# Kernel tuning notes

Hardware: AMD Instinct MI355X
Metric: run time of the kernel (lower is better)

Reference implementation:

```python
import jax, jax.numpy as jnp
import numpy as np

DIM = 512
HEADS = 8
SEQ = 2048
BATCH = 4


def setup_inputs() -> dict:
    key = jax.random.key(0)
    k = jax.random.split(key, 6)
    x = jax.random.normal(k[0], (BATCH, SEQ, DIM), dtype=jnp.float32)
    mask = jax.random.normal(k[1], (BATCH, SEQ, SEQ), dtype=jnp.float32)
    Wqkv = jax.random.normal(k[2], (3 * DIM, DIM), dtype=jnp.float32) * 0.02
    Btab = jax.random.normal(k[3], (1, HEADS, 2 * SEQ - 1), dtype=jnp.float32) * 0.02
    Wproj = jax.random.normal(k[4], (DIM, DIM), dtype=jnp.float32) * 0.02
    bproj = jax.random.normal(k[5], (DIM,), dtype=jnp.float32) * 0.02
    return {"x": x, "mask": mask, "Wqkv": Wqkv, "Btab": Btab,
            "Wproj": Wproj, "bproj": bproj}


def reference(x, mask, Wqkv, Btab, Wproj, bproj):
    B, N, C = x.shape
    H = Btab.shape[1]
    seq = (Btab.shape[2] + 1) // 2
    head_dim = C // H
    scale = head_dim ** (-0.5)

    # qkv projection (no bias), split into q,k,v of shape [B,H,N,head_dim]
    qkv = (x @ Wqkv.T).reshape(B, N, 3, H, head_dim)
    qkv = jnp.transpose(qkv, (2, 0, 3, 1, 4))  # [3,B,H,N,hd]
    q, k, v = qkv[0], qkv[1], qkv[2]

    # gathered relative-position bias: B_index[i,j] = i - j + seq - 1
    idx = jnp.arange(N)[:, None] - jnp.arange(N)[None, :] + (seq - 1)  # [N,N]
    bias = Btab[:, :, idx]  # [1,H,N,N]

    attn = jnp.einsum('bhnd,bhmd->bhnm', q, k) * scale + bias
    attn = attn + mask[:, None, :, :]  # additive mask, broadcast over heads
    attn = jax.nn.softmax(attn, axis=-1)

    out = jnp.einsum('bhnm,bhmd->bhnd', attn, v)  # [B,H,N,hd]
    out = jnp.transpose(out, (0, 2, 1, 3)).reshape(B, N, C)
    return out @ Wproj.T + bproj
```

## Files before the change

kernel.cpp:

```cpp
#include <hip/hip_runtime.h>


typedef __attribute__((ext_vector_type(8))) short short8;
typedef __attribute__((ext_vector_type(4))) float f32x4;

#define SEQ   2048
#define NHEAD 8
#define NBATCH 4
#define HD    64
#define CDIM  512

__device__ __forceinline__ unsigned short f32_to_bf16_rn(float f) {
  unsigned u = __builtin_bit_cast(unsigned, f);
  u += 0x7FFFu + ((u >> 16) & 1u);
  return (unsigned short)(u >> 16);
}

__global__ __launch_bounds__(256) void cvt_f32_bf16(const float* __restrict__ in,
                                                    ushort* __restrict__ out, int n4) {
  int i = blockIdx.x * 256 + threadIdx.x;
  const int stride = gridDim.x * 256;
  for (; i < n4; i += stride) {
    float4 v = reinterpret_cast<const float4*>(in)[i];
    ushort4 o;
    o.x = f32_to_bf16_rn(v.x);
    o.y = f32_to_bf16_rn(v.y);
    o.z = f32_to_bf16_rn(v.z);
    o.w = f32_to_bf16_rn(v.w);
    reinterpret_cast<ushort4*>(out)[i] = o;
  }
}

template <int MODE>
__global__ __launch_bounds__(256) void gemm_nt(
    const ushort* __restrict__ A, const ushort* __restrict__ Bm,
    ushort* __restrict__ qo, ushort* __restrict__ ko, ushort* __restrict__ vto,
    const float* __restrict__ bias, float* __restrict__ outf) {
  const int K = 512;
  __shared__ ushort As[128 * 40];
  __shared__ ushort Bs[128 * 40];

  const int t = threadIdx.x;
  const int bn = blockIdx.x, bm = blockIdx.y;
  const int lane = t & 63, w = t >> 6;
  const int wm = w >> 1, wn = w & 1;
  const int lr = lane & 15, lq = lane >> 4;
  const int m0 = bm * 128, n0 = bn * 128;

  f32x4 acc[4][4];
#pragma unroll
  for (int i = 0; i < 4; ++i)
#pragma unroll
    for (int j = 0; j < 4; ++j) acc[i][j] = (f32x4){0.f, 0.f, 0.f, 0.f};

  for (int kt = 0; kt < K; kt += 32) {
#pragma unroll
    for (int p = 0; p < 2; ++p) {
      const int flat = p * 256 + t;
      const int row = flat >> 2, seg = flat & 3;
      *(uint4*)&As[row * 40 + seg * 8] =
          *(const uint4*)(A + (size_t)(m0 + row) * K + kt + seg * 8);
      *(uint4*)&Bs[row * 40 + seg * 8] =
          *(const uint4*)(Bm + (size_t)(n0 + row) * K + kt + seg * 8);
    }
    __syncthreads();

    short8 af[4], bf[4];
#pragma unroll
    for (int i = 0; i < 4; ++i) {
      af[i] = *(const short8*)&As[(wm * 64 + i * 16 + lr) * 40 + lq * 8];
      bf[i] = *(const short8*)&Bs[(wn * 64 + i * 16 + lr) * 40 + lq * 8];
    }
#pragma unroll
    for (int i = 0; i < 4; ++i)
#pragma unroll
      for (int j = 0; j < 4; ++j)
        acc[i][j] = __builtin_amdgcn_mfma_f32_16x16x32_bf16(af[i], bf[j], acc[i][j], 0, 0, 0);
    __syncthreads();
  }

  if constexpr (MODE == 0) {
#pragma unroll
    for (int i = 0; i < 4; ++i) {
      const int mbase = m0 + wm * 64 + i * 16 + lq * 4;
      const int bb = mbase >> 11;
      const int s0 = mbase & 2047;
#pragma unroll
      for (int j = 0; j < 4; ++j) {
        const int nb = n0 + wn * 64 + j * 16;
        const int tt = nb >> 9;
        const int hh = (nb >> 6) & 7;
        const int d0 = nb & 63;
        const int bh = bb * NHEAD + hh;
        if (tt == 2) {
          ushort4 pk;
          pk.x = f32_to_bf16_rn(acc[i][j][0]);
          pk.y = f32_to_bf16_rn(acc[i][j][1]);
          pk.z = f32_to_bf16_rn(acc[i][j][2]);
          pk.w = f32_to_bf16_rn(acc[i][j][3]);
          *(ushort4*)(vto + ((size_t)bh * HD + d0 + lr) * SEQ + s0) = pk;
        } else {
          ushort* dst = (tt == 0) ? qo : ko;
#pragma unroll
          for (int r = 0; r < 4; ++r)
            dst[((size_t)bh * SEQ + s0 + r) * HD + d0 + lr] = f32_to_bf16_rn(acc[i][j][r]);
        }
      }
    }
  } else {
#pragma unroll
    for (int i = 0; i < 4; ++i) {
#pragma unroll
      for (int j = 0; j < 4; ++j) {
        const int n = n0 + wn * 64 + j * 16 + lr;
        const float bv = bias[n];
#pragma unroll
        for (int r = 0; r < 4; ++r) {
          const int m = m0 + wm * 64 + i * 16 + lq * 4 + r;
          outf[(size_t)m * 512 + n] = acc[i][j][r] + bv;
        }
      }
    }
  }
}

__global__ __launch_bounds__(128) void attn_fused(
    const ushort* __restrict__ Q, const ushort* __restrict__ Kt,
    const ushort* __restrict__ VT, const float* __restrict__ mask,
    const float* __restrict__ Btab, ushort* __restrict__ Out) {
  __shared__ ushort Ks[64 * 72];
  __shared__ ushort Vs[64 * 72];
  __shared__ ushort Ps[2][32 * 68];
  __shared__ ushort Bw[2112];

  const int flat = blockIdx.x;
  const int xcd = flat & 7;
  const int rr = flat >> 3;
  const int h = rr & 7;
  const int slot = rr >> 3;
  const int g = slot * 8 + xcd;
  const int qt = g & 31, b = g >> 5;

  const int bh = b * NHEAD + h;
  const ushort* qh = Q + (size_t)bh * SEQ * HD;
  const ushort* kh = Kt + (size_t)bh * SEQ * HD;
  const ushort* vh = VT + (size_t)bh * HD * SEQ;
  const float* mb = mask + (size_t)b * SEQ * SEQ;
  const float* bt = Btab + h * (2 * SEQ - 1);

  const int t = threadIdx.x;
  const int lane = t & 63, w = t >> 6;
  const int lr = lane & 15, lq = lane >> 4;
  const int qb0 = qt * 64;
  const int qbaseA = qb0 + w * 32;
  const int qbaseB = qbaseA + 16;

  for (int i = t; i < 2111; i += 128)
    Bw[i] = f32_to_bf16_rn(bt[qb0 + i] * 1.44269504f);

  short8 qfA0, qfA1, qfB0, qfB1;
  {
    const ushort* qpA = qh + (size_t)(qbaseA + lr) * HD + lq * 8;
    qfA0 = *(const short8*)qpA;
    qfA1 = *(const short8*)(qpA + 32);
    const ushort* qpB = qh + (size_t)(qbaseB + lr) * HD + lq * 8;
    qfB0 = *(const short8*)qpB;
    qfB1 = *(const short8*)(qpB + 32);
  }

  const float* mpA = mb + (size_t)(qbaseA + lq * 4) * SEQ + lr;
  const float* mpB = mb + (size_t)(qbaseB + lq * 4) * SEQ + lr;

  float lA0 = 0.f, lA1 = 0.f, lA2 = 0.f, lA3 = 0.f;
  float lB0 = 0.f, lB1 = 0.f, lB2 = 0.f, lB3 = 0.f;
  f32x4 ofA[4], ofB[4];
#pragma unroll
  for (int i = 0; i < 4; ++i) {
    ofA[i] = (f32x4){0.f, 0.f, 0.f, 0.f};
    ofB[i] = (f32x4){0.f, 0.f, 0.f, 0.f};
  }

  const int qrlA = w * 32 + lq * 4;
  const int srow = t >> 3;
  const int sseg = t & 7;

  const ushort* kp = kh + (size_t)srow * HD + sseg * 8;
  const ushort* vp = vh + (size_t)srow * SEQ + sseg * 8;

  uint4 kr0 = *(const uint4*)(kp);
  uint4 kr1 = *(const uint4*)(kp + 1024);
  uint4 kr2 = *(const uint4*)(kp + 2048);
  uint4 kr3 = *(const uint4*)(kp + 3072);
  uint4 vr0 = *(const uint4*)(vp);
  uint4 vr1 = *(const uint4*)(vp + 16 * SEQ);
  uint4 vr2 = *(const uint4*)(vp + 32 * SEQ);
  uint4 vr3 = *(const uint4*)(vp + 48 * SEQ);
  float mnA[4][4];
#pragma unroll
  for (int f = 0; f < 4; ++f)
#pragma unroll
    for (int r = 0; r < 4; ++r) mnA[f][r] = mpA[(size_t)r * SEQ + f * 16];

  for (int kv0 = 0; kv0 < SEQ; kv0 += 64) {
    __syncthreads();
    *(uint4*)&Ks[(srow)*72 + sseg * 8] = kr0;
    *(uint4*)&Ks[(16 + srow) * 72 + sseg * 8] = kr1;
    *(uint4*)&Ks[(32 + srow) * 72 + sseg * 8] = kr2;
    *(uint4*)&Ks[(48 + srow) * 72 + sseg * 8] = kr3;
    *(uint4*)&Vs[(srow)*72 + sseg * 8] = vr0;
    *(uint4*)&Vs[(16 + srow) * 72 + sseg * 8] = vr1;
    *(uint4*)&Vs[(32 + srow) * 72 + sseg * 8] = vr2;
    *(uint4*)&Vs[(48 + srow) * 72 + sseg * 8] = vr3;
    __syncthreads();

    const int nkv = (kv0 + 64 < SEQ) ? (kv0 + 64) : 0;

    float mnB[4][4];
#pragma unroll
    for (int f = 0; f < 4; ++f)
#pragma unroll
      for (int r = 0; r < 4; ++r) mnB[f][r] = mpB[(size_t)r * SEQ + kv0 + f * 16];

    f32x4 sfA[4], sfB[4];
#pragma unroll
    for (int f = 0; f < 4; ++f) {
      const ushort* kfp = &Ks[(f * 16 + lr) * 72 + lq * 8];
      const short8 k0 = *(const short8*)kfp;
      const short8 k1 = *(const short8*)(kfp + 32);
      sfA[f] = (f32x4){0.f, 0.f, 0.f, 0.f};
      sfA[f] = __builtin_amdgcn_mfma_f32_16x16x32_bf16(qfA0, k0, sfA[f], 0, 0, 0);
      sfA[f] = __builtin_amdgcn_mfma_f32_16x16x32_bf16(qfA1, k1, sfA[f], 0, 0, 0);
      sfB[f] = (f32x4){0.f, 0.f, 0.f, 0.f};
      sfB[f] = __builtin_amdgcn_mfma_f32_16x16x32_bf16(qfB0, k0, sfB[f], 0, 0, 0);
      sfB[f] = __builtin_amdgcn_mfma_f32_16x16x32_bf16(qfB1, k1, sfB[f], 0, 0, 0);
    }

#pragma unroll
    for (int f = 0; f < 4; ++f) {
      const int ib = qrlA - (kv0 + f * 16 + lr) + 2047;
#pragma unroll
      for (int r = 0; r < 4; ++r) {
        const float bw = __builtin_bit_cast(float, ((unsigned)Bw[ib + r]) << 16);
        const float xs = fmaf(sfA[f][r], 0.18033688f,
                              fmaf(mnA[f][r], 1.44269504f, bw));
        const float p = __builtin_amdgcn_exp2f(xs);
        if (r == 0) lA0 += p; else if (r == 1) lA1 += p;
        else if (r == 2) lA2 += p; else lA3 += p;
        const unsigned u = __builtin_bit_cast(unsigned, p);
        Ps[w][(lq * 4 + r) * 68 + f * 16 + lr] =
            (unsigned short)((u + 0x8000u) >> 16);
      }
    }

#pragma unroll
    for (int f = 0; f < 4; ++f)
#pragma unroll
      for (int r = 0; r < 4; ++r) mnA[f][r] = mpA[(size_t)r * SEQ + nkv + f * 16];

#pragma unroll
    for (int f = 0; f < 4; ++f) {
      const int ib = qrlA + 16 - (kv0 + f * 16 + lr) + 2047;
#pragma unroll
      for (int r = 0; r < 4; ++r) {
        const float bw = __builtin_bit_cast(float, ((unsigned)Bw[ib + r]) << 16);
        const float xs = fmaf(sfB[f][r], 0.18033688f,
                              fmaf(mnB[f][r], 1.44269504f, bw));
        const float p = __builtin_amdgcn_exp2f(xs);
        if (r == 0) lB0 += p; else if (r == 1) lB1 += p;
        else if (r == 2) lB2 += p; else lB3 += p;
        const unsigned u = __builtin_bit_cast(unsigned, p);
        Ps[w][(16 + lq * 4 + r) * 68 + f * 16 + lr] =
            (unsigned short)((u + 0x8000u) >> 16);
      }
    }

    kr0 = *(const uint4*)(kp + (size_t)nkv * HD);
    kr1 = *(const uint4*)(kp + (size_t)nkv * HD + 1024);
    kr2 = *(const uint4*)(kp + (size_t)nkv * HD + 2048);
    kr3 = *(const uint4*)(kp + (size_t)nkv * HD + 3072);
    vr0 = *(const uint4*)(vp + nkv);
    vr1 = *(const uint4*)(vp + nkv + 16 * SEQ);
    vr2 = *(const uint4*)(vp + nkv + 32 * SEQ);
    vr3 = *(const uint4*)(vp + nkv + 48 * SEQ);

#pragma unroll
    for (int ks = 0; ks < 2; ++ks) {
      union { uint2 u[2]; short8 s; } puA, puB;
      const int pbase = ks * 32 + lq * 8;
      puA.u[0] = *(const uint2*)&Ps[w][lr * 68 + pbase];
      puA.u[1] = *(const uint2*)&Ps[w][lr * 68 + pbase + 4];
      puB.u[0] = *(const uint2*)&Ps[w][(16 + lr) * 68 + pbase];
      puB.u[1] = *(const uint2*)&Ps[w][(16 + lr) * 68 + pbase + 4];
#pragma unroll
      for (int hf = 0; hf < 4; ++hf) {
        const short8 vf = *(const short8*)&Vs[(hf * 16 + lr) * 72 + ks * 32 + lq * 8];
        ofA[hf] = __builtin_amdgcn_mfma_f32_16x16x32_bf16(puA.s, vf, ofA[hf], 0, 0, 0);
        ofB[hf] = __builtin_amdgcn_mfma_f32_16x16x32_bf16(puB.s, vf, ofB[hf], 0, 0, 0);
      }
    }
  }

  float lA[4] = {lA0, lA1, lA2, lA3};
  float lB[4] = {lB0, lB1, lB2, lB3};
#pragma unroll
  for (int r = 0; r < 4; ++r) {
    float v = lA[r];
    v += __shfl_xor(v, 1); v += __shfl_xor(v, 2);
    v += __shfl_xor(v, 4); v += __shfl_xor(v, 8);
    lA[r] = v;
    float u = lB[r];
    u += __shfl_xor(u, 1); u += __shfl_xor(u, 2);
    u += __shfl_xor(u, 4); u += __shfl_xor(u, 8);
    lB[r] = u;
  }
#pragma unroll
  for (int r = 0; r < 4; ++r) {
    const float invA = 1.0f / lA[r];
    const int qrA = qbaseA + lq * 4 + r;
    ushort* opA = Out + ((size_t)(b * SEQ + qrA)) * CDIM + h * HD;
#pragma unroll
    for (int hf = 0; hf < 4; ++hf) opA[hf * 16 + lr] = f32_to_bf16_rn(ofA[hf][r] * invA);
    const float invB = 1.0f / lB[r];
    const int qrB = qbaseB + lq * 4 + r;
    ushort* opB = Out + ((size_t)(b * SEQ + qrB)) * CDIM + h * HD;
#pragma unroll
    for (int hf = 0; hf < 4; ++hf) opB[hf * 16 + lr] = f32_to_bf16_rn(ofB[hf][r] * invB);
  }
}

extern "C" void kernel_launch(void* const* d_in, const int* in_sizes, int n_in,
                              void* d_out, int out_size, void* d_ws, size_t ws_size,
                              hipStream_t stream) {
  const float* x     = (const float*)d_in[0];
  const float* mask  = (const float*)d_in[1];
  const float* Wqkv  = (const float*)d_in[2];
  const float* Btab  = (const float*)d_in[3];
  const float* Wproj = (const float*)d_in[4];
  const float* bproj = (const float*)d_in[5];
  float* out = (float*)d_out;

  char* ws = (char*)d_ws;
  const size_t SZ_X   = (size_t)NBATCH * SEQ * CDIM;
  const size_t SZ_QKV = (size_t)3 * CDIM * CDIM;
  const size_t SZ_PRJ = (size_t)CDIM * CDIM;
  const size_t SZ_HD  = (size_t)NBATCH * NHEAD * SEQ * HD;

  ushort* xb    = (ushort*)ws; ws += SZ_X * 2;
  ushort* wqkvb = (ushort*)ws; ws += SZ_QKV * 2;
  ushort* wprjb = (ushort*)ws; ws += SZ_PRJ * 2;
  ushort* qb    = (ushort*)ws; ws += SZ_HD * 2;
  ushort* kb    = (ushort*)ws; ws += SZ_HD * 2;
  ushort* vtb   = (ushort*)ws; ws += SZ_HD * 2;
  ushort* aob   = (ushort*)ws; ws += SZ_X * 2;

  {
    int n4 = (int)(SZ_X / 4);
    int g = (n4 + 255) / 256; if (g > 4096) g = 4096;
    cvt_f32_bf16<<<g, 256, 0, stream>>>(x, xb, n4);
  }
  {
    int n4 = (int)(SZ_QKV / 4);
    cvt_f32_bf16<<<(n4 + 255) / 256, 256, 0, stream>>>(Wqkv, wqkvb, n4);
  }
  {
    int n4 = (int)(SZ_PRJ / 4);
    cvt_f32_bf16<<<(n4 + 255) / 256, 256, 0, stream>>>(Wproj, wprjb, n4);
  }

  gemm_nt<0><<<dim3(12, 64), 256, 0, stream>>>(xb, wqkvb, qb, kb, vtb, nullptr, nullptr);

  attn_fused<<<dim3(1024), 128, 0, stream>>>(qb, kb, vtb, mask, Btab, aob);

  gemm_nt<1><<<dim3(4, 64), 256, 0, stream>>>(aob, wprjb, nullptr, nullptr, nullptr, bproj, out);
}
```

Baseline: 142.9 us.

## Double-buffer K/V tiles in LDS and widen attention blocks to 128 queries

Grows each attention block from two wavefronts (64 query rows) to four (128 query rows), so every K/V tile staged in LDS is shared by twice as many queries, and launches half as many blocks. The K/V LDS tiles are now double-buffered: the prefetched tile is written into the next buffer right after a single barrier and the global loads run two tiles ahead, which removes one __syncthreads per iteration. The aim is to cut K/V global traffic and barrier stalls. In exchange it uses more LDS per block and puts 512 blocks on the grid, which may lower occupancy or leave compute units unevenly loaded.

```diff
diff --git a/kernel.cpp b/kernel.cpp
--- a/kernel.cpp
+++ b/kernel.cpp
@@ -124,14 +124,14 @@
   }
 }
 
-__global__ __launch_bounds__(128) void attn_fused(
+__global__ __launch_bounds__(256) void attn_fused(
     const ushort* __restrict__ Q, const ushort* __restrict__ Kt,
     const ushort* __restrict__ VT, const float* __restrict__ mask,
     const float* __restrict__ Btab, ushort* __restrict__ Out) {
-  __shared__ ushort Ks[64 * 72];
-  __shared__ ushort Vs[64 * 72];
-  __shared__ ushort Ps[2][32 * 68];
-  __shared__ ushort Bw[2112];
+  __shared__ ushort Ks[2][64 * 72];
+  __shared__ ushort Vs[2][64 * 72];
+  __shared__ ushort Ps[4][32 * 68];
+  __shared__ ushort Bw[2176];
 
   const int flat = blockIdx.x;
   const int xcd = flat & 7;
@@ -139,7 +139,7 @@
   const int h = rr & 7;
   const int slot = rr >> 3;
   const int g = slot * 8 + xcd;
-  const int qt = g & 31, b = g >> 5;
+  const int qt = g & 15, b = g >> 4;
 
   const int bh = b * NHEAD + h;
   const ushort* qh = Q + (size_t)bh * SEQ * HD;
@@ -151,11 +151,11 @@
   const int t = threadIdx.x;
   const int lane = t & 63, w = t >> 6;
   const int lr = lane & 15, lq = lane >> 4;
-  const int qb0 = qt * 64;
+  const int qb0 = qt * 128;
   const int qbaseA = qb0 + w * 32;
   const int qbaseB = qbaseA + 16;
 
-  for (int i = t; i < 2111; i += 128)
+  for (int i = t; i < 2175; i += 256)
     Bw[i] = f32_to_bf16_rn(bt[qb0 + i] * 1.44269504f);
 
   short8 qfA0, qfA1, qfB0, qfB1;
@@ -168,8 +168,13 @@
     qfB1 = *(const short8*)(qpB + 32);
   }
 
-  const float* mpA = mb + (size_t)(qbaseA + lq * 4) * SEQ + lr;
-  const float* mpB = mb + (size_t)(qbaseB + lq * 4) * SEQ + lr;
+  const float* mrowA[4];
+  const float* mrowB[4];
+#pragma unroll
+  for (int r = 0; r < 4; ++r) {
+    mrowA[r] = mb + (size_t)(qbaseA + lq * 4 + r) * SEQ + lr;
+    mrowB[r] = mb + (size_t)(qbaseB + lq * 4 + r) * SEQ + lr;
+  }
 
   float lA0 = 0.f, lA1 = 0.f, lA2 = 0.f, lA3 = 0.f;
   float lB0 = 0.f, lB1 = 0.f, lB2 = 0.f, lB3 = 0.f;
@@ -188,43 +193,51 @@
   const ushort* vp = vh + (size_t)srow * SEQ + sseg * 8;
 
   uint4 kr0 = *(const uint4*)(kp);
-  uint4 kr1 = *(const uint4*)(kp + 1024);
-  uint4 kr2 = *(const uint4*)(kp + 2048);
-  uint4 kr3 = *(const uint4*)(kp + 3072);
+  uint4 kr1 = *(const uint4*)(kp + 32 * HD);
   uint4 vr0 = *(const uint4*)(vp);
-  uint4 vr1 = *(const uint4*)(vp + 16 * SEQ);
-  uint4 vr2 = *(const uint4*)(vp + 32 * SEQ);
-  uint4 vr3 = *(const uint4*)(vp + 48 * SEQ);
+  uint4 vr1 = *(const uint4*)(vp + 32 * SEQ);
+  *(uint4*)&Ks[0][srow * 72 + sseg * 8] = kr0;
+  *(uint4*)&Ks[0][(32 + srow) * 72 + sseg * 8] = kr1;
+  *(uint4*)&Vs[0][srow * 72 + sseg * 8] = vr0;
+  *(uint4*)&Vs[0][(32 + srow) * 72 + sseg * 8] = vr1;
+  kr0 = *(const uint4*)(kp + 64 * HD);
+  kr1 = *(const uint4*)(kp + 96 * HD);
+  vr0 = *(const uint4*)(vp + 64);
+  vr1 = *(const uint4*)(vp + 64 + 32 * SEQ);
+
   float mnA[4][4];
 #pragma unroll
   for (int f = 0; f < 4; ++f)
 #pragma unroll
-    for (int r = 0; r < 4; ++r) mnA[f][r] = mpA[(size_t)r * SEQ + f * 16];
-
-  for (int kv0 = 0; kv0 < SEQ; kv0 += 64) {
+    for (int r = 0; r < 4; ++r) mnA[f][r] = mrowA[r][f * 16];
+
+  for (int it = 0; it < 32; ++it) {
+    const int kv0 = it * 64;
+    const int cur = it & 1, nxt = cur ^ 1;
+
     __syncthreads();
-    *(uint4*)&Ks[(srow)*72 + sseg * 8] = kr0;
-    *(uint4*)&Ks[(16 + srow) * 72 + sseg * 8] = kr1;
-    *(uint4*)&Ks[(32 + srow) * 72 + sseg * 8] = kr2;
-    *(uint4*)&Ks[(48 + srow) * 72 + sseg * 8] = kr3;
-    *(uint4*)&Vs[(srow)*72 + sseg * 8] = vr0;
-    *(uint4*)&Vs[(16 + srow) * 72 + sseg * 8] = vr1;
-    *(uint4*)&Vs[(32 + srow) * 72 + sseg * 8] = vr2;
-    *(uint4*)&Vs[(48 + srow) * 72 + sseg * 8] = vr3;
-    __syncthreads();
-
-    const int nkv = (kv0 + 64 < SEQ) ? (kv0 + 64) : 0;
+
+    *(uint4*)&Ks[nxt][srow * 72 + sseg * 8] = kr0;
+    *(uint4*)&Ks[nxt][(32 + srow) * 72 + sseg * 8] = kr1;
+    *(uint4*)&Vs[nxt][srow * 72 + sseg * 8] = vr0;
+    *(uint4*)&Vs[nxt][(32 + srow) * 72 + sseg * 8] = vr1;
 
     float mnB[4][4];
 #pragma unroll
     for (int f = 0; f < 4; ++f)
 #pragma unroll
-      for (int r = 0; r < 4; ++r) mnB[f][r] = mpB[(size_t)r * SEQ + kv0 + f * 16];
+      for (int r = 0; r < 4; ++r) mnB[f][r] = mrowB[r][kv0 + f * 16];
+
+    const int lkv = (it + 2 < 32) ? (it + 2) * 64 : 0;
+    kr0 = *(const uint4*)(kp + (size_t)lkv * HD);
+    kr1 = *(const uint4*)(kp + (size_t)(lkv + 32) * HD);
+    vr0 = *(const uint4*)(vp + lkv);
+    vr1 = *(const uint4*)(vp + lkv + 32 * SEQ);
 
     f32x4 sfA[4], sfB[4];
 #pragma unroll
     for (int f = 0; f < 4; ++f) {
-      const ushort* kfp = &Ks[(f * 16 + lr) * 72 + lq * 8];
+      const ushort* kfp = &Ks[cur][(f * 16 + lr) * 72 + lq * 8];
       const short8 k0 = *(const short8*)kfp;
       const short8 k1 = *(const short8*)(kfp + 32);
       sfA[f] = (f32x4){0.f, 0.f, 0.f, 0.f};
@@ -252,10 +265,11 @@
       }
     }
 
+    const int mkv = (it + 1 < 32) ? (it + 1) * 64 : 0;
 #pragma unroll
     for (int f = 0; f < 4; ++f)
 #pragma unroll
-      for (int r = 0; r < 4; ++r) mnA[f][r] = mpA[(size_t)r * SEQ + nkv + f * 16];
+      for (int r = 0; r < 4; ++r) mnA[f][r] = mrowA[r][mkv + f * 16];
 
 #pragma unroll
     for (int f = 0; f < 4; ++f) {
@@ -274,15 +288,6 @@
       }
     }
 
-    kr0 = *(const uint4*)(kp + (size_t)nkv * HD);
-    kr1 = *(const uint4*)(kp + (size_t)nkv * HD + 1024);
-    kr2 = *(const uint4*)(kp + (size_t)nkv * HD + 2048);
-    kr3 = *(const uint4*)(kp + (size_t)nkv * HD + 3072);
-    vr0 = *(const uint4*)(vp + nkv);
-    vr1 = *(const uint4*)(vp + nkv + 16 * SEQ);
-    vr2 = *(const uint4*)(vp + nkv + 32 * SEQ);
-    vr3 = *(const uint4*)(vp + nkv + 48 * SEQ);
-
 #pragma unroll
     for (int ks = 0; ks < 2; ++ks) {
       union { uint2 u[2]; short8 s; } puA, puB;
@@ -293,7 +298,8 @@
       puB.u[1] = *(const uint2*)&Ps[w][(16 + lr) * 68 + pbase + 4];
 #pragma unroll
       for (int hf = 0; hf < 4; ++hf) {
-        const short8 vf = *(const short8*)&Vs[(hf * 16 + lr) * 72 + ks * 32 + lq * 8];
+        const short8 vf =
+            *(const short8*)&Vs[cur][(hf * 16 + lr) * 72 + ks * 32 + lq * 8];
         ofA[hf] = __builtin_amdgcn_mfma_f32_16x16x32_bf16(puA.s, vf, ofA[hf], 0, 0, 0);
         ofB[hf] = __builtin_amdgcn_mfma_f32_16x16x32_bf16(puB.s, vf, ofB[hf], 0, 0, 0);
       }
@@ -369,7 +375,7 @@
 
   gemm_nt<0><<<dim3(12, 64), 256, 0, stream>>>(xb, wqkvb, qb, kb, vtb, nullptr, nullptr);
 
-  attn_fused<<<dim3(1024), 128, 0, stream>>>(qb, kb, vtb, mask, Btab, aob);
+  attn_fused<<<dim3(512), 256, 0, stream>>>(qb, kb, vtb, mask, Btab, aob);
 
   gemm_nt<1><<<dim3(4, 64), 256, 0, stream>>>(aob, wprjb, nullptr, nullptr, nullptr, bproj, out);
 }
```

Result: slower. 146.4 us (+2.4%).
